# Kernel optimization log

Measured on AMD Instinct MI355X. Metric: run time of the kernel, lower is better.

## Reference

```python
import jax, jax.numpy as jnp
import numpy as np

NUM_HEADS = 12


def setup_inputs() -> dict:
    key = jax.random.key(0)
    k1, k2, k3 = jax.random.split(key, 3)
    B, S, D = 2, 2048, 768
    x = jax.random.normal(k1, (B, S, D), dtype=jnp.float32)
    # torch Linear init: normal(std=0.002) weights, zero bias; stored as [in, out]
    W_qkv = jax.random.normal(k2, (D, 3 * D), dtype=jnp.float32) * 0.002
    b_qkv = jnp.zeros((3 * D,), dtype=jnp.float32)
    W_vw = jax.random.normal(k3, (D, D), dtype=jnp.float32) * 0.002
    b_vw = jnp.zeros((D,), dtype=jnp.float32)
    mask = jnp.ones((B, S), dtype=jnp.int32)  # padding mask, all valid
    return {"x": x, "W_qkv": W_qkv, "b_qkv": b_qkv, "W_vw": W_vw, "b_vw": b_vw, "mask": mask}


def reference(x, W_qkv, b_qkv, W_vw, b_vw, mask):
    B, S, D = x.shape
    H = NUM_HEADS
    Dh = D // H
    qkv = (x @ W_qkv + b_qkv).reshape(B, S, 3, H, Dh)
    q, k, v = qkv[:, :, 0], qkv[:, :, 1], qkv[:, :, 2]
    # [B, H, S, S] attention scores (full matrix, as in original)
    w = jnp.einsum('bshd,bzhd->bhsz', q, k)
    w = w / jnp.sqrt(jnp.asarray(Dh, dtype=x.dtype))  # scale=True
    # log-mask trick: padding mask [B,1,1,S] * causal tril [1,1,S,S]
    causal = jnp.tril(jnp.ones((S, S), dtype=x.dtype))
    wholemask = mask.astype(x.dtype)[:, None, None, :] * causal[None, None]
    w = w + jnp.log(wholemask)
    w = jax.nn.softmax(w, axis=-1)
    vw = jnp.einsum('bhsz,bzhd->bshd', w, v).reshape(B, S, D)
    return vw @ W_vw + b_vw
```

## Files before the change

kernel.cpp:

```cpp
#include <hip/hip_runtime.h>
#include <hip/hip_bf16.h>
#include <cmath>
#include <cstddef>

#define B_    2
#define S_    2048
#define D_    768
#define H_    12
#define DH_   64
#define NQKV_ 2304

typedef __attribute__((ext_vector_type(8))) short  short8;
typedef __attribute__((ext_vector_type(4))) short  short4v;
typedef __attribute__((ext_vector_type(4))) float  floatx4;

__device__ __forceinline__ unsigned short f2bf(float f) {
    union { __hip_bfloat16 h; unsigned short u; } cv;
    cv.h = __float2bfloat16(f);
    return cv.u;
}

__device__ __forceinline__ void stage16(const unsigned short* g, unsigned short* ldsbase, int lane) {
#if __has_builtin(__builtin_amdgcn_global_load_lds)
    __builtin_amdgcn_global_load_lds(
        (const __attribute__((address_space(1))) unsigned int*)g,
        (__attribute__((address_space(3))) unsigned int*)ldsbase, 16, 0, 0);
#else
    *(short8*)(ldsbase + lane * 8) = *(const short8*)g;
#endif
}

__global__ void cvt_x_kernel(const float* __restrict__ x, unsigned short* __restrict__ xb)
{
    int i = (blockIdx.x * 256 + threadIdx.x) * 8;
    float4 a = *(const float4*)(x + i);
    float4 b = *(const float4*)(x + i + 4);
    short8 v;
    v[0] = (short)f2bf(a.x); v[1] = (short)f2bf(a.y);
    v[2] = (short)f2bf(a.z); v[3] = (short)f2bf(a.w);
    v[4] = (short)f2bf(b.x); v[5] = (short)f2bf(b.y);
    v[6] = (short)f2bf(b.z); v[7] = (short)f2bf(b.w);
    *(short8*)(xb + i) = v;
}

__global__ void cvt_w_kernel(const float* __restrict__ Wq, const float* __restrict__ Wv,
                             unsigned short* __restrict__ WqT, unsigned short* __restrict__ WvT)
{
    const int z = blockIdx.z;
    const int N = z ? D_ : NQKV_;
    if ((int)blockIdx.x * 32 >= N) return;
    const float* W = z ? Wv : Wq;
    unsigned short* WT = z ? WvT : WqT;

    __shared__ float t[32][33];
    const int tx = threadIdx.x, ty = threadIdx.y;
    const int n0 = blockIdx.x * 32, k0 = blockIdx.y * 32;
    #pragma unroll
    for (int i = 0; i < 4; ++i)
        t[ty + i * 8][tx] = W[(size_t)(k0 + ty + i * 8) * N + n0 + tx];
    __syncthreads();
    #pragma unroll
    for (int i = 0; i < 4; ++i)
        WT[(size_t)(n0 + ty + i * 8) * 768 + k0 + tx] = f2bf(t[tx][ty + i * 8]);
}

__global__ void vt_kernel(const unsigned short* __restrict__ V, unsigned short* __restrict__ VT)
{
    __shared__ unsigned short t[64][72];
    const int bh = blockIdx.x, s0 = blockIdx.y * 64;
    const unsigned short* src = V + ((size_t)bh * S_ + s0) * DH_;
    const int r = threadIdx.x >> 3, c = (threadIdx.x & 7) * 8;
    #pragma unroll
    for (int it = 0; it < 2; ++it)
        *(short8*)&t[r + it * 32][c] = *(const short8*)(src + (size_t)(r + it * 32) * DH_ + c);
    __syncthreads();
    #pragma unroll
    for (int it = 0; it < 2; ++it) {
        int d = r + it * 32;
        short8 v;
        #pragma unroll
        for (int i = 0; i < 8; ++i) v[i] = (short)t[c + i][d];
        *(short8*)(VT + ((size_t)bh * DH_ + d) * S_ + s0 + c) = v;
    }
}

__global__ __launch_bounds__(256, 2)
void mm_qkv_kernel(const unsigned short* __restrict__ A, const unsigned short* __restrict__ BT,
                   const float* __restrict__ bias,
                   unsigned short* __restrict__ Qo, unsigned short* __restrict__ Ko,
                   unsigned short* __restrict__ Vo)
{
    __shared__ unsigned short As[128][32];
    __shared__ unsigned short Bs[128][32];
    const int tid = threadIdx.x;
    const int wid = tid >> 6, lane = tid & 63;
    const int q = lane >> 4, ln = lane & 15;
    const int wm = (wid & 1) * 64, wn = (wid >> 1) * 64;
    const int m0 = blockIdx.y * 128, n0 = blockIdx.x * 128;
    const int lrow = wid * 16 + (lane >> 2);
    const int lcol = (lane & 3) * 8;
    const unsigned short* Ag = A  + (size_t)(m0 + lrow) * 768 + lcol;
    const unsigned short* Bg = BT + (size_t)(n0 + lrow) * 768 + lcol;

    floatx4 acc[4][4] = {};
    for (int k0 = 0; k0 < 768; k0 += 32) {
        __syncthreads();
        stage16(Ag + k0,            &As[wid * 16][0],      lane);
        stage16(Ag + k0 + 64 * 768, &As[64 + wid * 16][0], lane);
        stage16(Bg + k0,            &Bs[wid * 16][0],      lane);
        stage16(Bg + k0 + 64 * 768, &Bs[64 + wid * 16][0], lane);
        __syncthreads();
        short8 af[4], bf[4];
        #pragma unroll
        for (int mt = 0; mt < 4; ++mt) af[mt] = *(const short8*)&As[wm + mt * 16 + ln][q * 8];
        #pragma unroll
        for (int nt = 0; nt < 4; ++nt) bf[nt] = *(const short8*)&Bs[wn + nt * 16 + ln][q * 8];
        #pragma unroll
        for (int mt = 0; mt < 4; ++mt)
            #pragma unroll
            for (int nt = 0; nt < 4; ++nt)
                acc[mt][nt] = __builtin_amdgcn_mfma_f32_16x16x32_bf16(af[mt], bf[nt], acc[mt][nt], 0, 0, 0);
    }

    const int t = n0 / 768;
    unsigned short* __restrict__ dst = (t == 0) ? Qo : ((t == 1) ? Ko : Vo);
    const float qscale = (t == 0) ? 0.18033688011112042f : 1.0f;
    const int colb = n0 - t * 768 + wn;
    float bv[4];
    #pragma unroll
    for (int nt = 0; nt < 4; ++nt) bv[nt] = bias[n0 + wn + nt * 16 + ln];
    #pragma unroll
    for (int mt = 0; mt < 4; ++mt)
        #pragma unroll
        for (int r = 0; r < 4; ++r) {
            int row = m0 + wm + mt * 16 + q * 4 + r;
            int bb = row >> 11, s = row & 2047;
            #pragma unroll
            for (int nt = 0; nt < 4; ++nt) {
                int col = colb + nt * 16 + ln;
                int h = col >> 6, d = col & 63;
                dst[((size_t)(bb * H_ + h) * S_ + s) * DH_ + d] = f2bf((acc[mt][nt][r] + bv[nt]) * qscale);
            }
        }
}

__global__ __launch_bounds__(256, 2)
void flash16_kernel(const unsigned short* __restrict__ Qg, const unsigned short* __restrict__ Kg,
                    const unsigned short* __restrict__ VTg, const int* __restrict__ mask,
                    unsigned short* __restrict__ VW)
{
    __shared__ unsigned short Pl[4][64][40];
    __shared__ float Ol[64][68];
    __shared__ float li_s[4][64];

    const int tid = threadIdx.x;
    const int wid = tid >> 6, lane = tid & 63;
    const int q = lane >> 4, ln = lane & 15;
    const int bh = blockIdx.x % 24;
    const int j  = 31 - blockIdx.x / 24;
    const int b = bh / H_, h = bh % H_;
    const int r0 = j * 64;

    const unsigned short* Qb = Qg  + (size_t)bh * S_ * DH_;
    const unsigned short* Kb = Kg  + (size_t)bh * S_ * DH_;
    const unsigned short* Vt = VTg + (size_t)bh * DH_ * S_;
    const int* mb = mask + b * S_;

    short8 qf[4][2];
    #pragma unroll
    for (int rt = 0; rt < 4; ++rt)
        #pragma unroll
        for (int kk = 0; kk < 2; ++kk)
            qf[rt][kk] = *(const short8*)(Qb + (size_t)(r0 + rt * 16 + ln) * DH_ + kk * 32 + q * 8);

    floatx4 o[4][4] = {};
    float li[4] = {};
    const int T = 2 * j + 2;

    for (int t = wid; t < T; t += 4) {
        const int z0 = t * 32;

        short8 kf[2][2];
        #pragma unroll
        for (int zt = 0; zt < 2; ++zt)
            #pragma unroll
            for (int kk = 0; kk < 2; ++kk)
                kf[zt][kk] = *(const short8*)(Kb + (size_t)(z0 + zt * 16 + ln) * DH_ + kk * 32 + q * 8);

        short8 vb[4];
        #pragma unroll
        for (int dt = 0; dt < 4; ++dt)
            vb[dt] = *(const short8*)(Vt + (size_t)(dt * 16 + ln) * S_ + z0 + q * 8);

        const int mi = mb[z0 + (lane & 31)];

        floatx4 s[2][4] = {};
        __builtin_amdgcn_s_setprio(1);
        #pragma unroll
        for (int zt = 0; zt < 2; ++zt)
            #pragma unroll
            for (int rt = 0; rt < 4; ++rt) {
                s[zt][rt] = __builtin_amdgcn_mfma_f32_16x16x32_bf16(kf[zt][0], qf[rt][0], s[zt][rt], 0, 0, 0);
                s[zt][rt] = __builtin_amdgcn_mfma_f32_16x16x32_bf16(kf[zt][1], qf[rt][1], s[zt][rt], 0, 0, 0);
            }
        __builtin_amdgcn_s_setprio(0);

        const bool diag = (z0 + 31 > r0);
        if (__all(mi != 0) && !diag) {
            #pragma unroll
            for (int zt = 0; zt < 2; ++zt)
                #pragma unroll
                for (int rt = 0; rt < 4; ++rt) {
                    float p0 = exp2f(s[zt][rt][0]);
                    float p1 = exp2f(s[zt][rt][1]);
                    float p2 = exp2f(s[zt][rt][2]);
                    float p3 = exp2f(s[zt][rt][3]);
                    li[rt] += (p0 + p1) + (p2 + p3);
                    short4v pk;
                    pk[0] = (short)f2bf(p0); pk[1] = (short)f2bf(p1);
                    pk[2] = (short)f2bf(p2); pk[3] = (short)f2bf(p3);
                    *(short4v*)&Pl[wid][rt * 16 + ln][zt * 16 + q * 4] = pk;
                }
        } else {
            const int4 mA = *(const int4*)&mb[z0 + q * 4];
            const int4 mB = *(const int4*)&mb[z0 + 16 + q * 4];
            int ma[2][4];
            ma[0][0] = mA.x; ma[0][1] = mA.y; ma[0][2] = mA.z; ma[0][3] = mA.w;
            ma[1][0] = mB.x; ma[1][1] = mB.y; ma[1][2] = mB.z; ma[1][3] = mB.w;
            #pragma unroll
            for (int zt = 0; zt < 2; ++zt)
                #pragma unroll
                for (int rt = 0; rt < 4; ++rt) {
                    const int zb = z0 + zt * 16 + q * 4;
                    const int r  = r0 + rt * 16 + ln;
                    float p[4];
                    #pragma unroll
                    for (int rr = 0; rr < 4; ++rr) {
                        p[rr] = exp2f(s[zt][rt][rr]);
                        if (!ma[zt][rr] || (zb + rr > r)) p[rr] = 0.0f;
                    }
                    li[rt] += (p[0] + p[1]) + (p[2] + p[3]);
                    short4v pk;
                    pk[0] = (short)f2bf(p[0]); pk[1] = (short)f2bf(p[1]);
                    pk[2] = (short)f2bf(p[2]); pk[3] = (short)f2bf(p[3]);
                    *(short4v*)&Pl[wid][rt * 16 + ln][zt * 16 + q * 4] = pk;
                }
        }

        #pragma unroll
        for (int mt = 0; mt < 4; ++mt) {
            short8 a = *(const short8*)&Pl[wid][mt * 16 + ln][q * 8];
            __builtin_amdgcn_s_setprio(1);
            #pragma unroll
            for (int dt = 0; dt < 4; ++dt)
                o[mt][dt] = __builtin_amdgcn_mfma_f32_16x16x32_bf16(a, vb[dt], o[mt][dt], 0, 0, 0);
            __builtin_amdgcn_s_setprio(0);
        }
    }

    #pragma unroll
    for (int rt = 0; rt < 4; ++rt) {
        float v = li[rt];
        v += __shfl_xor(v, 16);
        v += __shfl_xor(v, 32);
        li[rt] = v;
    }
    if (lane < 16) {
        #pragma unroll
        for (int rt = 0; rt < 4; ++rt)
            li_s[wid][rt * 16 + lane] = li[rt];
    }

    #pragma unroll
    for (int w = 0; w < 4; ++w) {
        if (wid == w) {
            #pragma unroll
            for (int mt = 0; mt < 4; ++mt)
                #pragma unroll
                for (int r = 0; r < 4; ++r) {
                    int row = mt * 16 + q * 4 + r;
                    #pragma unroll
                    for (int dt = 0; dt < 4; ++dt) {
                        if (w == 0) Ol[row][dt * 16 + ln]  = o[mt][dt][r];
                        else        Ol[row][dt * 16 + ln] += o[mt][dt][r];
                    }
                }
        }
        __syncthreads();
    }

    #pragma unroll
    for (int it = 0; it < 2; ++it) {
        int idx = tid + it * 256;
        int row = idx >> 3, c = (idx & 7) * 8;
        float inv = 1.0f / (li_s[0][row] + li_s[1][row] + li_s[2][row] + li_s[3][row]);
        short8 ov;
        #pragma unroll
        for (int i = 0; i < 8; ++i) ov[i] = (short)f2bf(Ol[row][c + i] * inv);
        *(short8*)(VW + ((size_t)b * S_ + r0 + row) * D_ + h * DH_ + c) = ov;
    }
}

__global__ __launch_bounds__(256, 2)
void mm_proj_kernel(const unsigned short* __restrict__ A, const unsigned short* __restrict__ BT,
                    const float* __restrict__ bias, float* __restrict__ C)
{
    __shared__ unsigned short As[128][32];
    __shared__ unsigned short Bs[64][32];
    const int tid = threadIdx.x;
    const int wid = tid >> 6, lane = tid & 63;
    const int q = lane >> 4, ln = lane & 15;
    const int wm = (wid & 1) * 64, wn = (wid >> 1) * 32;
    const int m0 = blockIdx.y * 128, n0 = blockIdx.x * 64;
    const int lrow = wid * 16 + (lane >> 2);
    const int lcol = (lane & 3) * 8;
    const unsigned short* Ag = A  + (size_t)(m0 + lrow) * 768 + lcol;
    const unsigned short* Bg = BT + (size_t)(n0 + lrow) * 768 + lcol;

    floatx4 acc[4][2] = {};
    for (int k0 = 0; k0 < 768; k0 += 32) {
        __syncthreads();
        stage16(Ag + k0,            &As[wid * 16][0],      lane);
        stage16(Ag + k0 + 64 * 768, &As[64 + wid * 16][0], lane);
        stage16(Bg + k0,            &Bs[wid * 16][0],      lane);
        __syncthreads();
        short8 af[4], bf[2];
        #pragma unroll
        for (int mt = 0; mt < 4; ++mt) af[mt] = *(const short8*)&As[wm + mt * 16 + ln][q * 8];
        #pragma unroll
        for (int nt = 0; nt < 2; ++nt) bf[nt] = *(const short8*)&Bs[wn + nt * 16 + ln][q * 8];
        #pragma unroll
        for (int mt = 0; mt < 4; ++mt)
            #pragma unroll
            for (int nt = 0; nt < 2; ++nt)
                acc[mt][nt] = __builtin_amdgcn_mfma_f32_16x16x32_bf16(af[mt], bf[nt], acc[mt][nt], 0, 0, 0);
    }

    float bv[2];
    #pragma unroll
    for (int nt = 0; nt < 2; ++nt) bv[nt] = bias[n0 + wn + nt * 16 + ln];
    #pragma unroll
    for (int mt = 0; mt < 4; ++mt)
        #pragma unroll
        for (int r = 0; r < 4; ++r) {
            size_t row = (size_t)m0 + wm + mt * 16 + q * 4 + r;
            #pragma unroll
            for (int nt = 0; nt < 2; ++nt)
                C[row * D_ + n0 + wn + nt * 16 + ln] = acc[mt][nt][r] + bv[nt];
        }
}

extern "C" void kernel_launch(void* const* d_in, const int* in_sizes, int n_in,
                              void* d_out, int out_size, void* d_ws, size_t ws_size,
                              hipStream_t stream)
{
    (void)in_sizes; (void)n_in; (void)out_size; (void)ws_size;
    const float* x    = (const float*)d_in[0];
    const float* Wqkv = (const float*)d_in[1];
    const float* bqkv = (const float*)d_in[2];
    const float* Wvw  = (const float*)d_in[3];
    const float* bvw  = (const float*)d_in[4];
    const int*   mask = (const int*)d_in[5];
    float* out = (float*)d_out;

    const size_t XN  = (size_t)B_ * S_ * D_;
    unsigned short* ws  = (unsigned short*)d_ws;
    unsigned short* xb  = ws;
    unsigned short* WqT = xb  + XN;
    unsigned short* WvT = WqT + (size_t)NQKV_ * D_;
    unsigned short* Qb  = WvT + (size_t)D_ * D_;
    unsigned short* Kb  = Qb + XN;
    unsigned short* Vb  = Kb + XN;
    unsigned short* VbT = Vb + XN;
    unsigned short* VW  = VbT + XN;

    cvt_x_kernel<<<dim3(XN / (256 * 8)), 256, 0, stream>>>(x, xb);
    cvt_w_kernel<<<dim3(NQKV_ / 32, D_ / 32, 2), dim3(32, 8), 0, stream>>>(Wqkv, Wvw, WqT, WvT);
    mm_qkv_kernel<<<dim3(NQKV_ / 128, (B_ * S_) / 128), 256, 0, stream>>>(xb, WqT, bqkv, Qb, Kb, Vb);
    vt_kernel<<<dim3(B_ * H_, S_ / 64), 256, 0, stream>>>(Vb, VbT);
    flash16_kernel<<<dim3(24 * 32), 256, 0, stream>>>(Qb, Kb, VbT, mask, VW);
    mm_proj_kernel<<<dim3(D_ / 64, (B_ * S_) / 128), 256, 0, stream>>>(VW, WvT, bvw, out);
}
```

Measured before the change: 163.0 us.

## Process two 64-row query tiles per 512-thread flash block with aliased LDS

```diff
diff --git a/kernel.cpp b/kernel.cpp
--- a/kernel.cpp
+++ b/kernel.cpp
@@ -144,22 +144,26 @@
         }
 }
 
-__global__ __launch_bounds__(256, 2)
-void flash16_kernel(const unsigned short* __restrict__ Qg, const unsigned short* __restrict__ Kg,
+__global__ __launch_bounds__(512, 2)
+void flash18_kernel(const unsigned short* __restrict__ Qg, const unsigned short* __restrict__ Kg,
                     const unsigned short* __restrict__ VTg, const int* __restrict__ mask,
                     unsigned short* __restrict__ VW)
 {
-    __shared__ unsigned short Pl[4][64][40];
-    __shared__ float Ol[64][68];
-    __shared__ float li_s[4][64];
+    __shared__ __align__(16) unsigned char smem[40960];
+    unsigned short (*Pl)[64][40] = (unsigned short (*)[64][40])smem;
+    float (*Ol)[64][68]  = (float (*)[64][68])smem;
+    float (*li_s)[4][64] = (float (*)[4][64])(smem + 34816);
 
     const int tid = threadIdx.x;
     const int wid = tid >> 6, lane = tid & 63;
     const int q = lane >> 4, ln = lane & 15;
+    const int tm = wid >> 2;
+    const int kw = wid & 3;
     const int bh = blockIdx.x % 24;
-    const int j  = 31 - blockIdx.x / 24;
+    const int j  = 15 - blockIdx.x / 24;
     const int b = bh / H_, h = bh % H_;
-    const int r0 = j * 64;
+    const int r0t = j * 128 + tm * 64;
+    const int T   = (r0t + 63) / 32 + 1;
 
     const unsigned short* Qb = Qg  + (size_t)bh * S_ * DH_;
     const unsigned short* Kb = Kg  + (size_t)bh * S_ * DH_;
@@ -171,13 +175,12 @@
     for (int rt = 0; rt < 4; ++rt)
         #pragma unroll
         for (int kk = 0; kk < 2; ++kk)
-            qf[rt][kk] = *(const short8*)(Qb + (size_t)(r0 + rt * 16 + ln) * DH_ + kk * 32 + q * 8);
+            qf[rt][kk] = *(const short8*)(Qb + (size_t)(r0t + rt * 16 + ln) * DH_ + kk * 32 + q * 8);
 
     floatx4 o[4][4] = {};
     float li[4] = {};
-    const int T = 2 * j + 2;
-
-    for (int t = wid; t < T; t += 4) {
+
+    for (int t = kw; t < T; t += 4) {
         const int z0 = t * 32;
 
         short8 kf[2][2];
@@ -205,7 +208,7 @@
             }
         __builtin_amdgcn_s_setprio(0);
 
-        const bool diag = (z0 + 31 > r0);
+        const bool diag = (z0 + 31 > r0t);
         if (__all(mi != 0) && !diag) {
             #pragma unroll
             for (int zt = 0; zt < 2; ++zt)
@@ -232,7 +235,7 @@
                 #pragma unroll
                 for (int rt = 0; rt < 4; ++rt) {
                     const int zb = z0 + zt * 16 + q * 4;
-                    const int r  = r0 + rt * 16 + ln;
+                    const int r  = r0t + rt * 16 + ln;
                     float p[4];
                     #pragma unroll
                     for (int rr = 0; rr < 4; ++rr) {
@@ -265,15 +268,18 @@
         v += __shfl_xor(v, 32);
         li[rt] = v;
     }
+
+    __syncthreads();
+
     if (lane < 16) {
         #pragma unroll
         for (int rt = 0; rt < 4; ++rt)
-            li_s[wid][rt * 16 + lane] = li[rt];
+            li_s[tm][kw][rt * 16 + lane] = li[rt];
     }
 
     #pragma unroll
     for (int w = 0; w < 4; ++w) {
-        if (wid == w) {
+        if (kw == w) {
             #pragma unroll
             for (int mt = 0; mt < 4; ++mt)
                 #pragma unroll
@@ -281,8 +287,8 @@
                     int row = mt * 16 + q * 4 + r;
                     #pragma unroll
                     for (int dt = 0; dt < 4; ++dt) {
-                        if (w == 0) Ol[row][dt * 16 + ln]  = o[mt][dt][r];
-                        else        Ol[row][dt * 16 + ln] += o[mt][dt][r];
+                        if (w == 0) Ol[tm][row][dt * 16 + ln]  = o[mt][dt][r];
+                        else        Ol[tm][row][dt * 16 + ln] += o[mt][dt][r];
                     }
                 }
         }
@@ -291,13 +297,15 @@
 
     #pragma unroll
     for (int it = 0; it < 2; ++it) {
-        int idx = tid + it * 256;
+        int idx = tid + it * 512;
         int row = idx >> 3, c = (idx & 7) * 8;
-        float inv = 1.0f / (li_s[0][row] + li_s[1][row] + li_s[2][row] + li_s[3][row]);
+        int tmw = row >> 6, lr = row & 63;
+        float inv = 1.0f / (li_s[tmw][0][lr] + li_s[tmw][1][lr] +
+                            li_s[tmw][2][lr] + li_s[tmw][3][lr]);
         short8 ov;
         #pragma unroll
-        for (int i = 0; i < 8; ++i) ov[i] = (short)f2bf(Ol[row][c + i] * inv);
-        *(short8*)(VW + ((size_t)b * S_ + r0 + row) * D_ + h * DH_ + c) = ov;
+        for (int i = 0; i < 8; ++i) ov[i] = (short)f2bf(Ol[tmw][lr][c + i] * inv);
+        *(short8*)(VW + ((size_t)b * S_ + j * 128 + row) * D_ + h * DH_ + c) = ov;
     }
 }
 
@@ -378,6 +386,6 @@
     cvt_w_kernel<<<dim3(NQKV_ / 32, D_ / 32, 2), dim3(32, 8), 0, stream>>>(Wqkv, Wvw, WqT, WvT);
     mm_qkv_kernel<<<dim3(NQKV_ / 128, (B_ * S_) / 128), 256, 0, stream>>>(xb, WqT, bqkv, Qb, Kb, Vb);
     vt_kernel<<<dim3(B_ * H_, S_ / 64), 256, 0, stream>>>(Vb, VbT);
-    flash16_kernel<<<dim3(24 * 32), 256, 0, stream>>>(Qb, Kb, VbT, mask, VW);
+    flash18_kernel<<<dim3(24 * 16), 512, 0, stream>>>(Qb, Kb, VbT, mask, VW);
     mm_proj_kernel<<<dim3(D_ / 64, (B_ * S_) / 128), 256, 0, stream>>>(VW, WvT, bvw, out);
 }
```

Measured after the change: 164.0 us. Within noise of the previous version (+0.6%).

## Pair causal query tiles per block and use 8 waves per block

Applied to the files above, without the earlier changes.

```diff
diff --git a/kernel.cpp b/kernel.cpp
--- a/kernel.cpp
+++ b/kernel.cpp
@@ -144,160 +144,168 @@
         }
 }
 
-__global__ __launch_bounds__(256, 2)
-void flash16_kernel(const unsigned short* __restrict__ Qg, const unsigned short* __restrict__ Kg,
+__global__ __launch_bounds__(512, 2)
+void flash20_kernel(const unsigned short* __restrict__ Qg, const unsigned short* __restrict__ Kg,
                     const unsigned short* __restrict__ VTg, const int* __restrict__ mask,
                     unsigned short* __restrict__ VW)
 {
-    __shared__ unsigned short Pl[4][64][40];
-    __shared__ float Ol[64][68];
-    __shared__ float li_s[4][64];
+    __shared__ __align__(16) unsigned char smem[40960];
+    unsigned short (*Pl)[64][40] = (unsigned short (*)[64][40])smem;
+    float (*Ol)[68]  = (float (*)[68])smem;
+    float (*li_s)[64] = (float (*)[64])(smem + 17408);
 
     const int tid = threadIdx.x;
     const int wid = tid >> 6, lane = tid & 63;
     const int q = lane >> 4, ln = lane & 15;
     const int bh = blockIdx.x % 24;
-    const int j  = 31 - blockIdx.x / 24;
+    const int p  = blockIdx.x / 24;
     const int b = bh / H_, h = bh % H_;
-    const int r0 = j * 64;
 
     const unsigned short* Qb = Qg  + (size_t)bh * S_ * DH_;
     const unsigned short* Kb = Kg  + (size_t)bh * S_ * DH_;
     const unsigned short* Vt = VTg + (size_t)bh * DH_ * S_;
     const int* mb = mask + b * S_;
 
-    short8 qf[4][2];
-    #pragma unroll
-    for (int rt = 0; rt < 4; ++rt)
-        #pragma unroll
-        for (int kk = 0; kk < 2; ++kk)
-            qf[rt][kk] = *(const short8*)(Qb + (size_t)(r0 + rt * 16 + ln) * DH_ + kk * 32 + q * 8);
-
-    floatx4 o[4][4] = {};
-    float li[4] = {};
-    const int T = 2 * j + 2;
-
-    for (int t = wid; t < T; t += 4) {
-        const int z0 = t * 32;
-
-        short8 kf[2][2];
-        #pragma unroll
-        for (int zt = 0; zt < 2; ++zt)
+    for (int ph = 0; ph < 2; ++ph) {
+        const int j  = ph ? p : (31 - p);
+        const int r0 = j * 64;
+        const int T  = 2 * j + 2;
+
+        short8 qf[4][2];
+        #pragma unroll
+        for (int rt = 0; rt < 4; ++rt)
             #pragma unroll
             for (int kk = 0; kk < 2; ++kk)
-                kf[zt][kk] = *(const short8*)(Kb + (size_t)(z0 + zt * 16 + ln) * DH_ + kk * 32 + q * 8);
-
-        short8 vb[4];
-        #pragma unroll
-        for (int dt = 0; dt < 4; ++dt)
-            vb[dt] = *(const short8*)(Vt + (size_t)(dt * 16 + ln) * S_ + z0 + q * 8);
-
-        const int mi = mb[z0 + (lane & 31)];
-
-        floatx4 s[2][4] = {};
-        __builtin_amdgcn_s_setprio(1);
-        #pragma unroll
-        for (int zt = 0; zt < 2; ++zt)
-            #pragma unroll
-            for (int rt = 0; rt < 4; ++rt) {
-                s[zt][rt] = __builtin_amdgcn_mfma_f32_16x16x32_bf16(kf[zt][0], qf[rt][0], s[zt][rt], 0, 0, 0);
-                s[zt][rt] = __builtin_amdgcn_mfma_f32_16x16x32_bf16(kf[zt][1], qf[rt][1], s[zt][rt], 0, 0, 0);
+                qf[rt][kk] = *(const short8*)(Qb + (size_t)(r0 + rt * 16 + ln) * DH_ + kk * 32 + q * 8);
+
+        floatx4 o[4][4] = {};
+        float li[4] = {};
+
+        for (int t = wid; t < T; t += 8) {
+            const int z0 = t * 32;
+
+            short8 kf[2][2];
+            #pragma unroll
+            for (int zt = 0; zt < 2; ++zt)
+                #pragma unroll
+                for (int kk = 0; kk < 2; ++kk)
+                    kf[zt][kk] = *(const short8*)(Kb + (size_t)(z0 + zt * 16 + ln) * DH_ + kk * 32 + q * 8);
+
+            short8 vb[4];
+            #pragma unroll
+            for (int dt = 0; dt < 4; ++dt)
+                vb[dt] = *(const short8*)(Vt + (size_t)(dt * 16 + ln) * S_ + z0 + q * 8);
+
+            const int mi = mb[z0 + (lane & 31)];
+
+            floatx4 s[2][4] = {};
+            __builtin_amdgcn_s_setprio(1);
+            #pragma unroll
+            for (int zt = 0; zt < 2; ++zt)
+                #pragma unroll
+                for (int rt = 0; rt < 4; ++rt) {
+                    s[zt][rt] = __builtin_amdgcn_mfma_f32_16x16x32_bf16(kf[zt][0], qf[rt][0], s[zt][rt], 0, 0, 0);
+                    s[zt][rt] = __builtin_amdgcn_mfma_f32_16x16x32_bf16(kf[zt][1], qf[rt][1], s[zt][rt], 0, 0, 0);
+                }
+            __builtin_amdgcn_s_setprio(0);
+
+            const bool diag = (z0 + 31 > r0);
+            if (__all(mi != 0) && !diag) {
+                #pragma unroll
+                for (int zt = 0; zt < 2; ++zt)
+                    #pragma unroll
+                    for (int rt = 0; rt < 4; ++rt) {
+                        float p0 = exp2f(s[zt][rt][0]);
+                        float p1 = exp2f(s[zt][rt][1]);
+                        float p2 = exp2f(s[zt][rt][2]);
+                        float p3 = exp2f(s[zt][rt][3]);
+                        li[rt] += (p0 + p1) + (p2 + p3);
+                        short4v pk;
+                        pk[0] = (short)f2bf(p0); pk[1] = (short)f2bf(p1);
+                        pk[2] = (short)f2bf(p2); pk[3] = (short)f2bf(p3);
+                        *(short4v*)&Pl[wid][rt * 16 + ln][zt * 16 + q * 4] = pk;
+                    }
+            } else {
+                const int4 mA = *(const int4*)&mb[z0 + q * 4];
+                const int4 mB = *(const int4*)&mb[z0 + 16 + q * 4];
+                int ma[2][4];
+                ma[0][0] = mA.x; ma[0][1] = mA.y; ma[0][2] = mA.z; ma[0][3] = mA.w;
+                ma[1][0] = mB.x; ma[1][1] = mB.y; ma[1][2] = mB.z; ma[1][3] = mB.w;
+                #pragma unroll
+                for (int zt = 0; zt < 2; ++zt)
+                    #pragma unroll
+                    for (int rt = 0; rt < 4; ++rt) {
+                        const int zb = z0 + zt * 16 + q * 4;
+                        const int r  = r0 + rt * 16 + ln;
+                        float pv[4];
+                        #pragma unroll
+                        for (int rr = 0; rr < 4; ++rr) {
+                            pv[rr] = exp2f(s[zt][rt][rr]);
+                            if (!ma[zt][rr] || (zb + rr > r)) pv[rr] = 0.0f;
+                        }
+                        li[rt] += (pv[0] + pv[1]) + (pv[2] + pv[3]);
+                        short4v pk;
+                        pk[0] = (short)f2bf(pv[0]); pk[1] = (short)f2bf(pv[1]);
+                        pk[2] = (short)f2bf(pv[2]); pk[3] = (short)f2bf(pv[3]);
+                        *(short4v*)&Pl[wid][rt * 16 + ln][zt * 16 + q * 4] = pk;
+                    }
             }
-        __builtin_amdgcn_s_setprio(0);
-
-        const bool diag = (z0 + 31 > r0);
-        if (__all(mi != 0) && !diag) {
-            #pragma unroll
-            for (int zt = 0; zt < 2; ++zt)
-                #pragma unroll
-                for (int rt = 0; rt < 4; ++rt) {
-                    float p0 = exp2f(s[zt][rt][0]);
-                    float p1 = exp2f(s[zt][rt][1]);
-                    float p2 = exp2f(s[zt][rt][2]);
-                    float p3 = exp2f(s[zt][rt][3]);
-                    li[rt] += (p0 + p1) + (p2 + p3);
-                    short4v pk;
-                    pk[0] = (short)f2bf(p0); pk[1] = (short)f2bf(p1);
-                    pk[2] = (short)f2bf(p2); pk[3] = (short)f2bf(p3);
-                    *(short4v*)&Pl[wid][rt * 16 + ln][zt * 16 + q * 4] = pk;
-                }
-        } else {
-            const int4 mA = *(const int4*)&mb[z0 + q * 4];
-            const int4 mB = *(const int4*)&mb[z0 + 16 + q * 4];
-            int ma[2][4];
-            ma[0][0] = mA.x; ma[0][1] = mA.y; ma[0][2] = mA.z; ma[0][3] = mA.w;
-            ma[1][0] = mB.x; ma[1][1] = mB.y; ma[1][2] = mB.z; ma[1][3] = mB.w;
-            #pragma unroll
-            for (int zt = 0; zt < 2; ++zt)
-                #pragma unroll
-                for (int rt = 0; rt < 4; ++rt) {
-                    const int zb = z0 + zt * 16 + q * 4;
-                    const int r  = r0 + rt * 16 + ln;
-                    float p[4];
+
+            #pragma unroll
+            for (int mt = 0; mt < 4; ++mt) {
+                short8 a = *(const short8*)&Pl[wid][mt * 16 + ln][q * 8];
+                __builtin_amdgcn_s_setprio(1);
+                #pragma unroll
+                for (int dt = 0; dt < 4; ++dt)
+                    o[mt][dt] = __builtin_amdgcn_mfma_f32_16x16x32_bf16(a, vb[dt], o[mt][dt], 0, 0, 0);
+                __builtin_amdgcn_s_setprio(0);
+            }
+        }
+
+        #pragma unroll
+        for (int rt = 0; rt < 4; ++rt) {
+            float v = li[rt];
+            v += __shfl_xor(v, 16);
+            v += __shfl_xor(v, 32);
+            li[rt] = v;
+        }
+
+        __syncthreads();
+
+        if (lane < 16) {
+            #pragma unroll
+            for (int rt = 0; rt < 4; ++rt)
+                li_s[wid][rt * 16 + lane] = li[rt];
+        }
+
+        #pragma unroll
+        for (int w = 0; w < 8; ++w) {
+            if (wid == w) {
+                #pragma unroll
+                for (int mt = 0; mt < 4; ++mt)
                     #pragma unroll
-                    for (int rr = 0; rr < 4; ++rr) {
-                        p[rr] = exp2f(s[zt][rt][rr]);
-                        if (!ma[zt][rr] || (zb + rr > r)) p[rr] = 0.0f;
+                    for (int r = 0; r < 4; ++r) {
+                        int row = mt * 16 + q * 4 + r;
+                        #pragma unroll
+                        for (int dt = 0; dt < 4; ++dt) {
+                            if (w == 0) Ol[row][dt * 16 + ln]  = o[mt][dt][r];
+                            else        Ol[row][dt * 16 + ln] += o[mt][dt][r];
+                        }
                     }
-                    li[rt] += (p[0] + p[1]) + (p[2] + p[3]);
-                    short4v pk;
-                    pk[0] = (short)f2bf(p[0]); pk[1] = (short)f2bf(p[1]);
-                    pk[2] = (short)f2bf(p[2]); pk[3] = (short)f2bf(p[3]);
-                    *(short4v*)&Pl[wid][rt * 16 + ln][zt * 16 + q * 4] = pk;
-                }
-        }
-
-        #pragma unroll
-        for (int mt = 0; mt < 4; ++mt) {
-            short8 a = *(const short8*)&Pl[wid][mt * 16 + ln][q * 8];
-            __builtin_amdgcn_s_setprio(1);
-            #pragma unroll
-            for (int dt = 0; dt < 4; ++dt)
-                o[mt][dt] = __builtin_amdgcn_mfma_f32_16x16x32_bf16(a, vb[dt], o[mt][dt], 0, 0, 0);
-            __builtin_amdgcn_s_setprio(0);
-        }
-    }
-
-    #pragma unroll
-    for (int rt = 0; rt < 4; ++rt) {
-        float v = li[rt];
-        v += __shfl_xor(v, 16);
-        v += __shfl_xor(v, 32);
-        li[rt] = v;
-    }
-    if (lane < 16) {
-        #pragma unroll
-        for (int rt = 0; rt < 4; ++rt)
-            li_s[wid][rt * 16 + lane] = li[rt];
-    }
-
-    #pragma unroll
-    for (int w = 0; w < 4; ++w) {
-        if (wid == w) {
-            #pragma unroll
-            for (int mt = 0; mt < 4; ++mt)
-                #pragma unroll
-                for (int r = 0; r < 4; ++r) {
-                    int row = mt * 16 + q * 4 + r;
-                    #pragma unroll
-                    for (int dt = 0; dt < 4; ++dt) {
-                        if (w == 0) Ol[row][dt * 16 + ln]  = o[mt][dt][r];
-                        else        Ol[row][dt * 16 + ln] += o[mt][dt][r];
-                    }
-                }
-        }
-        __syncthreads();
-    }
-
-    #pragma unroll
-    for (int it = 0; it < 2; ++it) {
-        int idx = tid + it * 256;
-        int row = idx >> 3, c = (idx & 7) * 8;
-        float inv = 1.0f / (li_s[0][row] + li_s[1][row] + li_s[2][row] + li_s[3][row]);
-        short8 ov;
-        #pragma unroll
-        for (int i = 0; i < 8; ++i) ov[i] = (short)f2bf(Ol[row][c + i] * inv);
-        *(short8*)(VW + ((size_t)b * S_ + r0 + row) * D_ + h * DH_ + c) = ov;
+            }
+            __syncthreads();
+        }
+
+        {
+            int row = tid >> 3, c = (tid & 7) * 8;
+            float inv = 1.0f / (li_s[0][row] + li_s[1][row] + li_s[2][row] + li_s[3][row] +
+                                li_s[4][row] + li_s[5][row] + li_s[6][row] + li_s[7][row]);
+            short8 ov;
+            #pragma unroll
+            for (int i = 0; i < 8; ++i) ov[i] = (short)f2bf(Ol[row][c + i] * inv);
+            *(short8*)(VW + ((size_t)b * S_ + r0 + row) * D_ + h * DH_ + c) = ov;
+        }
+        __syncthreads();
     }
 }
 
@@ -378,6 +386,6 @@
     cvt_w_kernel<<<dim3(NQKV_ / 32, D_ / 32, 2), dim3(32, 8), 0, stream>>>(Wqkv, Wvw, WqT, WvT);
     mm_qkv_kernel<<<dim3(NQKV_ / 128, (B_ * S_) / 128), 256, 0, stream>>>(xb, WqT, bqkv, Qb, Kb, Vb);
     vt_kernel<<<dim3(B_ * H_, S_ / 64), 256, 0, stream>>>(Vb, VbT);
-    flash16_kernel<<<dim3(24 * 32), 256, 0, stream>>>(Qb, Kb, VbT, mask, VW);
+    flash20_kernel<<<dim3(24 * 16), 512, 0, stream>>>(Qb, Kb, VbT, mask, VW);
     mm_proj_kernel<<<dim3(D_ / 64, (B_ * S_) / 128), 256, 0, stream>>>(VW, WvT, bvw, out);
 }
```

Result: slower. 188.3 us (+15.5%).
